# Performance work log

Hardware: AMD Instinct MI355X
Metric: run time of the kernel (lower is better)

The kernel has to match this reference:

```python
import jax, jax.numpy as jnp
import numpy as np

EPS = 1e-5
N, E, G = 65536, 262144, 256
DV, DE, DG = 256, 128, 256


def _ln(x):
    # LayerNorm without affine over the last dim
    mu = jnp.mean(x, axis=-1, keepdims=True)
    var = jnp.mean(jnp.square(x - mu), axis=-1, keepdims=True)
    return (x - mu) * jax.lax.rsqrt(var + EPS)


def setup_inputs() -> dict:
    key = jax.random.key(0)
    ks = jax.random.split(key, 14)
    inp = {
        'fv': jax.random.normal(ks[0], (N, DV), jnp.float32),
        'fe': jax.random.normal(ks[1], (E, DE), jnp.float32),
        'fg': jax.random.normal(ks[2], (G, DG), jnp.float32),
        'fv_pos': jax.random.normal(ks[3], (N, 3), jnp.float32),
        'fv_c': jax.random.normal(ks[4], (N, DV), jnp.float32),
        'fe_c': jax.random.normal(ks[5], (E, DE), jnp.float32),
        'fv_pos_c': jax.random.normal(ks[6], (N, DV), jnp.float32),
        # learned params (original zero-inits the modulation Linears; we use
        # small random weights so the kernel path is exercised)
        'W_v': jax.random.normal(ks[7], (2 * DV, DV), jnp.float32) * 0.02,
        'b_v': jnp.zeros((2 * DV,), jnp.float32),
        'W_vpos': jax.random.normal(ks[8], (DE, DV), jnp.float32) * 0.02,
        'b_vpos': jnp.zeros((DE,), jnp.float32),
        'W_e': jax.random.normal(ks[9], (2 * DE, DE), jnp.float32) * 0.02,
        'b_e': jnp.zeros((2 * DE,), jnp.float32),
        'g_gamma': jnp.ones((DG,), jnp.float32),
        'g_beta': jnp.zeros((DG,), jnp.float32),
        'W_pos': jax.random.normal(ks[10], (1, DG), jnp.float32) * 0.02,
        'b_pos': jnp.zeros((1,), jnp.float32),
        'src': jax.random.randint(ks[11], (E,), 0, N, jnp.int32),
        'dst': jax.random.randint(ks[12], (E,), 0, N, jnp.int32),
        'node_gid': (jnp.arange(N, dtype=jnp.int32) // (N // G)),
    }
    return inp


def reference(fv, fe, fg, fv_pos, fv_c, fe_c, fv_pos_c,
              W_v, b_v, W_vpos, b_vpos, W_e, b_e,
              g_gamma, g_beta, W_pos, b_pos,
              src, dst, node_gid):
    act = jax.nn.silu
    # --- node modulation ---
    mod_v = act(fv_c + fv_pos_c) @ W_v.T + b_v            # [N, 2*DV]
    shift_v, scale_v = jnp.split(mod_v, 2, axis=1)
    fv_out = _ln(fv) * (1.0 + scale_v) + shift_v
    # --- edge modulation with gsddmm('add') gather ---
    fvp = fv_pos_c @ W_vpos.T + b_vpos                    # [N, DE]
    fv2e = fvp[src] + fvp[dst]                            # sddmm add [E, DE]
    mod_e = act(fe_c + fv2e) @ W_e.T + b_e                # [E, 2*DE]
    shift_e, scale_e = jnp.split(mod_e, 2, axis=1)
    fe_out = _ln(fe) * (1.0 + scale_e) + shift_e
    # --- adaptive position scale-norm (per-graph, equivariant) ---
    ones = jnp.ones((N,), fv_pos.dtype)
    cnt = jax.ops.segment_sum(ones, node_gid, num_segments=G)          # [G]
    mean = jax.ops.segment_sum(fv_pos, node_gid, num_segments=G) / cnt[:, None]
    centered = fv_pos - mean[node_gid]                                  # [N, 3]
    sq = jax.ops.segment_sum(jnp.sum(jnp.square(centered), axis=1), node_gid, num_segments=G)
    rms = jnp.sqrt(sq / (cnt * 3.0) + EPS)                              # [G]
    pos_n = centered / rms[node_gid][:, None]
    s = act(fg) @ W_pos.T + b_pos                                       # [G, 1]
    fv_pos_out = pos_n * (1.0 + s)[node_gid]
    # --- graph LayerNorm (affine) ---
    fg_out = _ln(fg) * g_gamma + g_beta
    return (fv_out, fe_out, fg_out, fv_pos_out)
```

## Files before the change

kernel.cpp:

```cpp
#include <hip/hip_runtime.h>

#define N_NODES 65536
#define N_EDGES 262144
#define N_GRAPH 256
#define DV 256
#define DE 128
#define DG 256
#define EPS 1e-5f

typedef __bf16 bf16_t;
typedef bf16_t bf16x8 __attribute__((ext_vector_type(8)));
typedef float f32x4 __attribute__((ext_vector_type(4)));
typedef unsigned short ushort_t;

__device__ __forceinline__ float silu_f(float x) {
  return x / (1.0f + __expf(-x));
}
__device__ __forceinline__ unsigned short f2bf(float f) {
  unsigned int u = __float_as_uint(f);
  u += 0x7fffu + ((u >> 16) & 1u);
  return (unsigned short)(u >> 16);
}
__device__ __forceinline__ float bf2f(unsigned short h) {
  return __uint_as_float(((unsigned int)h) << 16);
}
__device__ __forceinline__ void split_bf(float x, ushort_t& hi, ushort_t& lo) {
  hi = f2bf(x);
  lo = f2bf(x - bf2f(hi));
}
__device__ __forceinline__ void wave_reduce2(float& s1, float& s2) {
  #pragma unroll
  for (int off = 32; off > 0; off >>= 1) {
    s1 += __shfl_xor(s1, off);
    s2 += __shfl_xor(s2, off);
  }
}

__global__ __launch_bounds__(256) void k_prep(
    const float* __restrict__ W_v, const float* __restrict__ W_e,
    const float* __restrict__ W_vpos, ushort_t* __restrict__ Wv_bf,
    ushort_t* __restrict__ We_bf, ushort_t* __restrict__ Wvpos_bf) {
  int idx = blockIdx.x * 256 + threadIdx.x;
  const float* s;
  ushort_t* d;
  int o;
  if (idx < 32768) { s = W_v; d = Wv_bf; o = idx; }
  else if (idx < 40960) { s = W_e; d = We_bf; o = idx - 32768; }
  else { s = W_vpos; d = Wvpos_bf; o = idx - 40960; }
  float4 v = *(const float4*)&s[(size_t)o * 4];
  ushort4 r;
  r.x = f2bf(v.x); r.y = f2bf(v.y); r.z = f2bf(v.z); r.w = f2bf(v.w);
  *(ushort4*)&d[(size_t)o * 4] = r;
}

__global__ __launch_bounds__(512) void k_fvp(
    const float* __restrict__ fv_pos_c, const ushort_t* __restrict__ Wvpos_bf,
    const float* __restrict__ b_vpos, ushort_t* __restrict__ fvp_bf) {
  __shared__ __align__(16) ushort_t Xh[32][264];
  __shared__ __align__(16) ushort_t Xl[32][264];
  const int tid = threadIdx.x;
  const int l = tid & 63, w = tid >> 6;
  const int m0 = blockIdx.x * 32;
  #pragma unroll
  for (int i = 0; i < 4; ++i) {
    int idx = i * 512 + tid;
    int r = idx >> 6, c4 = idx & 63;
    float4 v = *(const float4*)&fv_pos_c[(size_t)(m0 + r) * DV + c4 * 4];
    ushort4 h, lo;
    split_bf(v.x, h.x, lo.x);
    split_bf(v.y, h.y, lo.y);
    split_bf(v.z, h.z, lo.z);
    split_bf(v.w, h.w, lo.w);
    *(ushort4*)&Xh[r][c4 * 4] = h;
    *(ushort4*)&Xl[r][c4 * 4] = lo;
  }
  __syncthreads();
  f32x4 acc[2];
  acc[0] = (f32x4)(0.f);
  acc[1] = (f32x4)(0.f);
  const int mrow = (w & 1) * 16;
  const int ncol0 = (w >> 1) * 32;
  const int arow = mrow + (l & 15);
  for (int kc = 0; kc < 8; ++kc) {
    int ke = kc * 32 + (l >> 4) * 8;
    bf16x8 ah = *(const bf16x8*)&Xh[arow][ke];
    bf16x8 al = *(const bf16x8*)&Xl[arow][ke];
    #pragma unroll
    for (int ni = 0; ni < 2; ++ni) {
      bf16x8 b = *(const bf16x8*)&Wvpos_bf[(size_t)(ncol0 + ni * 16 + (l & 15)) * DV + ke];
      acc[ni] = __builtin_amdgcn_mfma_f32_16x16x32_bf16(al, b, acc[ni], 0, 0, 0);
      acc[ni] = __builtin_amdgcn_mfma_f32_16x16x32_bf16(ah, b, acc[ni], 0, 0, 0);
    }
  }
  #pragma unroll
  for (int ni = 0; ni < 2; ++ni) {
    int col = ncol0 + ni * 16 + (l & 15);
    float bias = b_vpos[col];
    #pragma unroll
    for (int j = 0; j < 4; ++j) {
      int row = m0 + mrow + (l >> 4) * 4 + j;
      fvp_bf[(size_t)row * DE + col] = f2bf(acc[ni][j] + bias);
    }
  }
}

__global__ __launch_bounds__(512) void k_node(
    const float* __restrict__ fv, const float* __restrict__ fv_c,
    const float* __restrict__ fv_pos_c, const ushort_t* __restrict__ Wv_bf,
    const float* __restrict__ b_v, float* __restrict__ fv_out) {
  __shared__ __align__(16) ushort_t Xh[32][264];
  __shared__ __align__(16) ushort_t Xl[32][264];
  __shared__ float muL[32], rsL[32];
  const int tid = threadIdx.x;
  const int l = tid & 63, w = tid >> 6;
  const int m0 = blockIdx.x * 32;
  #pragma unroll
  for (int i = 0; i < 4; ++i) {
    int idx = i * 512 + tid;
    int r = idx >> 6, c4 = idx & 63;
    size_t g = (size_t)(m0 + r) * DV + c4 * 4;
    float4 a = *(const float4*)&fv_c[g];
    float4 b = *(const float4*)&fv_pos_c[g];
    ushort4 h, lo;
    split_bf(silu_f(a.x + b.x), h.x, lo.x);
    split_bf(silu_f(a.y + b.y), h.y, lo.y);
    split_bf(silu_f(a.z + b.z), h.z, lo.z);
    split_bf(silu_f(a.w + b.w), h.w, lo.w);
    *(ushort4*)&Xh[r][c4 * 4] = h;
    *(ushort4*)&Xl[r][c4 * 4] = lo;
  }
  #pragma unroll
  for (int rr = 0; rr < 4; ++rr) {
    int row = w * 4 + rr;
    float4 v = *(const float4*)&fv[(size_t)(m0 + row) * DV + l * 4];
    float s1 = v.x + v.y + v.z + v.w;
    float s2 = v.x * v.x + v.y * v.y + v.z * v.z + v.w * v.w;
    wave_reduce2(s1, s2);
    if (l == 0) {
      float mu = s1 * (1.0f / DV);
      float var = s2 * (1.0f / DV) - mu * mu;
      muL[row] = mu;
      rsL[row] = rsqrtf(var + EPS);
    }
  }
  __syncthreads();
  f32x4 acc[2][4];
  #pragma unroll
  for (int mi = 0; mi < 2; ++mi)
    #pragma unroll
    for (int ni = 0; ni < 4; ++ni) acc[mi][ni] = (f32x4)(0.f);
  int ncol[4];
  ncol[0] = w * 32;
  ncol[1] = w * 32 + 16;
  ncol[2] = DV + w * 32;
  ncol[3] = DV + w * 32 + 16;
  for (int kc = 0; kc < 8; ++kc) {
    int ke = kc * 32 + (l >> 4) * 8;
    bf16x8 ah[2], al[2];
    #pragma unroll
    for (int mi = 0; mi < 2; ++mi) {
      ah[mi] = *(const bf16x8*)&Xh[mi * 16 + (l & 15)][ke];
      al[mi] = *(const bf16x8*)&Xl[mi * 16 + (l & 15)][ke];
    }
    #pragma unroll
    for (int ni = 0; ni < 4; ++ni) {
      bf16x8 b = *(const bf16x8*)&Wv_bf[(size_t)(ncol[ni] + (l & 15)) * DV + ke];
      #pragma unroll
      for (int mi = 0; mi < 2; ++mi) {
        acc[mi][ni] = __builtin_amdgcn_mfma_f32_16x16x32_bf16(al[mi], b, acc[mi][ni], 0, 0, 0);
        acc[mi][ni] = __builtin_amdgcn_mfma_f32_16x16x32_bf16(ah[mi], b, acc[mi][ni], 0, 0, 0);
      }
    }
  }
  #pragma unroll
  for (int ni2 = 0; ni2 < 2; ++ni2) {
    int c = w * 32 + ni2 * 16 + (l & 15);
    float bsh = b_v[c];
    float bsc = b_v[DV + c];
    #pragma unroll
    for (int mi = 0; mi < 2; ++mi)
      #pragma unroll
      for (int j = 0; j < 4; ++j) {
        int row = mi * 16 + (l >> 4) * 4 + j;
        size_t g = (size_t)(m0 + row) * DV + c;
        float v = fv[g];
        float sh = acc[mi][ni2][j] + bsh;
        float sc = acc[mi][ni2 + 2][j] + bsc;
        fv_out[g] = (v - muL[row]) * rsL[row] * (1.0f + sc) + sh;
      }
  }
}

__global__ __launch_bounds__(512) void k_edge(
    const float* __restrict__ fe, const float* __restrict__ fe_c,
    const ushort_t* __restrict__ fvp_bf, const int* __restrict__ src,
    const int* __restrict__ dst, const ushort_t* __restrict__ We_bf,
    const float* __restrict__ b_e, float* __restrict__ fe_out) {
  __shared__ __align__(16) ushort_t Xh[64][136];
  __shared__ __align__(16) ushort_t Xl[64][136];
  __shared__ float muL[64], rsL[64];
  const int tid = threadIdx.x;
  const int l = tid & 63, w = tid >> 6;
  const int m0 = blockIdx.x * 64;
  const int sub = l & 15, quad = l >> 4;
  #pragma unroll
  for (int i = 0; i < 4; ++i) {
    int idx = i * 512 + tid;
    int r = idx >> 5, c4 = idx & 31;
    int sr = src[m0 + r], dr = dst[m0 + r];
    float4 a = *(const float4*)&fe_c[(size_t)(m0 + r) * DE + c4 * 4];
    ushort4 p = *(const ushort4*)&fvp_bf[(size_t)sr * DE + c4 * 4];
    ushort4 q = *(const ushort4*)&fvp_bf[(size_t)dr * DE + c4 * 4];
    ushort4 h, lo;
    split_bf(silu_f(a.x + bf2f(p.x) + bf2f(q.x)), h.x, lo.x);
    split_bf(silu_f(a.y + bf2f(p.y) + bf2f(q.y)), h.y, lo.y);
    split_bf(silu_f(a.z + bf2f(p.z) + bf2f(q.z)), h.z, lo.z);
    split_bf(silu_f(a.w + bf2f(p.w) + bf2f(q.w)), h.w, lo.w);
    *(ushort4*)&Xh[r][c4 * 4] = h;
    *(ushort4*)&Xl[r][c4 * 4] = lo;
  }
  #pragma unroll
  for (int j2 = 0; j2 < 2; ++j2) {
    int row = w * 8 + quad * 2 + j2;
    float s1 = 0.f, s2 = 0.f;
    #pragma unroll
    for (int ci = 0; ci < 8; ++ci) {
      float v = fe[(size_t)(m0 + row) * DE + ci * 16 + sub];
      s1 += v;
      s2 += v * v;
    }
    #pragma unroll
    for (int off = 1; off < 16; off <<= 1) {
      s1 += __shfl_xor(s1, off);
      s2 += __shfl_xor(s2, off);
    }
    if (sub == 0) {
      float m = s1 * (1.0f / DE);
      float var = s2 * (1.0f / DE) - m * m;
      muL[row] = m;
      rsL[row] = rsqrtf(var + EPS);
    }
  }
  __syncthreads();
  f32x4 acc[4][2];
  #pragma unroll
  for (int mi = 0; mi < 4; ++mi) {
    acc[mi][0] = (f32x4)(0.f);
    acc[mi][1] = (f32x4)(0.f);
  }
  for (int kc = 0; kc < 4; ++kc) {
    int ke = kc * 32 + quad * 8;
    bf16x8 ah[4], al[4];
    #pragma unroll
    for (int mi = 0; mi < 4; ++mi) {
      ah[mi] = *(const bf16x8*)&Xh[mi * 16 + sub][ke];
      al[mi] = *(const bf16x8*)&Xl[mi * 16 + sub][ke];
    }
    #pragma unroll
    for (int ni = 0; ni < 2; ++ni) {
      bf16x8 b = *(const bf16x8*)&We_bf[(size_t)(ni * DE + w * 16 + sub) * DE + ke];
      #pragma unroll
      for (int mi = 0; mi < 4; ++mi) {
        acc[mi][ni] = __builtin_amdgcn_mfma_f32_16x16x32_bf16(al[mi], b, acc[mi][ni], 0, 0, 0);
        acc[mi][ni] = __builtin_amdgcn_mfma_f32_16x16x32_bf16(ah[mi], b, acc[mi][ni], 0, 0, 0);
      }
    }
  }
  {
    int c = w * 16 + sub;
    float bsh = b_e[c];
    float bsc = b_e[DE + c];
    #pragma unroll
    for (int mi = 0; mi < 4; ++mi)
      #pragma unroll
      for (int j = 0; j < 4; ++j) {
        int row = mi * 16 + quad * 4 + j;
        size_t g = (size_t)(m0 + row) * DE + c;
        float v = fe[g];
        float sh = acc[mi][0][j] + bsh;
        float sc = acc[mi][1][j] + bsc;
        fe_out[g] = (v - muL[row]) * rsL[row] * (1.0f + sc) + sh;
      }
  }
}

__global__ __launch_bounds__(256) void k_fg_pos(
    const float* __restrict__ fg, const float* __restrict__ g_gamma,
    const float* __restrict__ g_beta, const float* __restrict__ W_pos,
    const float* __restrict__ b_pos, const float* __restrict__ fv_pos,
    const int* __restrict__ node_gid, float* __restrict__ fg_out,
    float* __restrict__ pos_out) {
  const int g = blockIdx.x, t = threadIdx.x;
  const int lane = t & 63, wave = t >> 6;
  __shared__ float p1[4], p2[4], p3[4];
  __shared__ float px[4], py[4], pz[4], pq[4];
  float x = fg[g * DG + t];
  float sv = silu_f(x) * W_pos[t];
  float s1 = x, s2 = x * x, s3 = sv;
  #pragma unroll
  for (int off = 32; off > 0; off >>= 1) {
    s1 += __shfl_xor(s1, off);
    s2 += __shfl_xor(s2, off);
    s3 += __shfl_xor(s3, off);
  }
  if (lane == 0) { p1[wave] = s1; p2[wave] = s2; p3[wave] = s3; }
  __syncthreads();
  s1 = p1[0] + p1[1] + p1[2] + p1[3];
  s2 = p2[0] + p2[1] + p2[2] + p2[3];
  float mu = s1 * (1.0f / DG);
  float var = s2 * (1.0f / DG) - mu * mu;
  float rstd = rsqrtf(var + EPS);
  fg_out[g * DG + t] = (x - mu) * rstd * g_gamma[t] + g_beta[t];
  float s_own = (p3[0] + p3[1] + p3[2] + p3[3]) + b_pos[0];
  const int i = g * 256 + t;
  const int gid = node_gid[i];
  float vx = fv_pos[3 * i + 0];
  float vy = fv_pos[3 * i + 1];
  float vz = fv_pos[3 * i + 2];
  if (__syncthreads_and(gid == g)) {
    float rx = vx, ry = vy, rz = vz, rq = vx * vx + vy * vy + vz * vz;
    #pragma unroll
    for (int off = 32; off > 0; off >>= 1) {
      rx += __shfl_xor(rx, off);
      ry += __shfl_xor(ry, off);
      rz += __shfl_xor(rz, off);
      rq += __shfl_xor(rq, off);
    }
    if (lane == 0) { px[wave] = rx; py[wave] = ry; pz[wave] = rz; pq[wave] = rq; }
    __syncthreads();
    float sx = px[0] + px[1] + px[2] + px[3];
    float sy = py[0] + py[1] + py[2] + py[3];
    float sz = pz[0] + pz[1] + pz[2] + pz[3];
    float sq = pq[0] + pq[1] + pq[2] + pq[3];
    float ic = 1.0f / 256.0f;
    float mx = sx * ic, my = sy * ic, mz = sz * ic;
    float cq = fmaxf(sq - 256.0f * (mx * mx + my * my + mz * mz), 0.0f);
    float rms = sqrtf(cq / (256.0f * 3.0f) + EPS);
    float sc = (1.0f + s_own) / rms;
    pos_out[3 * i + 0] = (vx - mx) * sc;
    pos_out[3 * i + 1] = (vy - my) * sc;
    pos_out[3 * i + 2] = (vz - mz) * sc;
  } else {
    float sx = 0.f, sy = 0.f, sz = 0.f, sq = 0.f, cnt = 0.f;
    for (int j = 0; j < N_NODES; ++j) {
      if (node_gid[j] == gid) {
        float ax = fv_pos[3 * j + 0];
        float ay = fv_pos[3 * j + 1];
        float az = fv_pos[3 * j + 2];
        sx += ax; sy += ay; sz += az;
        sq += ax * ax + ay * ay + az * az;
        cnt += 1.0f;
      }
    }
    float ic = 1.0f / fmaxf(cnt, 1.0f);
    float mx = sx * ic, my = sy * ic, mz = sz * ic;
    float cq = fmaxf(sq - cnt * (mx * mx + my * my + mz * mz), 0.0f);
    float rms = sqrtf(cq / (cnt * 3.0f) + EPS);
    float sg = 0.f;
    for (int c = 0; c < DG; ++c) sg += silu_f(fg[gid * DG + c]) * W_pos[c];
    float sc = (1.0f + sg + b_pos[0]) / rms;
    pos_out[3 * i + 0] = (vx - mx) * sc;
    pos_out[3 * i + 1] = (vy - my) * sc;
    pos_out[3 * i + 2] = (vz - mz) * sc;
  }
}

extern "C" void kernel_launch(void* const* d_in, const int* in_sizes, int n_in,
                              void* d_out, int out_size, void* d_ws,
                              size_t ws_size, hipStream_t stream) {
  const float* fv = (const float*)d_in[0];
  const float* fe = (const float*)d_in[1];
  const float* fg = (const float*)d_in[2];
  const float* fv_pos = (const float*)d_in[3];
  const float* fv_c = (const float*)d_in[4];
  const float* fe_c = (const float*)d_in[5];
  const float* fv_pos_c = (const float*)d_in[6];
  const float* W_v = (const float*)d_in[7];
  const float* b_v = (const float*)d_in[8];
  const float* W_vpos = (const float*)d_in[9];
  const float* b_vpos = (const float*)d_in[10];
  const float* W_e = (const float*)d_in[11];
  const float* b_e = (const float*)d_in[12];
  const float* g_gamma = (const float*)d_in[13];
  const float* g_beta = (const float*)d_in[14];
  const float* W_pos = (const float*)d_in[15];
  const float* b_pos = (const float*)d_in[16];
  const int* src = (const int*)d_in[17];
  const int* dst = (const int*)d_in[18];
  const int* node_gid = (const int*)d_in[19];

  float* out = (float*)d_out;
  float* fv_out = out;
  float* fe_out = fv_out + (size_t)N_NODES * DV;
  float* fg_out = fe_out + (size_t)N_EDGES * DE;
  float* pos_out = fg_out + (size_t)N_GRAPH * DG;

  char* ws = (char*)d_ws;
  ushort_t* fvp_bf = (ushort_t*)ws;
  ushort_t* Wv_bf = (ushort_t*)(ws + 16777216);
  ushort_t* We_bf = (ushort_t*)(ws + 16777216 + 262144);
  ushort_t* Wvpos_bf = (ushort_t*)(ws + 16777216 + 262144 + 65536);

  k_prep<<<192, 256, 0, stream>>>(W_v, W_e, W_vpos, Wv_bf, We_bf, Wvpos_bf);
  k_fvp<<<N_NODES / 32, 512, 0, stream>>>(fv_pos_c, Wvpos_bf, b_vpos, fvp_bf);
  k_node<<<N_NODES / 32, 512, 0, stream>>>(fv, fv_c, fv_pos_c, Wv_bf, b_v, fv_out);
  k_edge<<<N_EDGES / 64, 512, 0, stream>>>(fe, fe_c, fvp_bf, src, dst, We_bf,
                                           b_e, fe_out);
  k_fg_pos<<<N_GRAPH, 256, 0, stream>>>(fg, g_gamma, g_beta, W_pos, b_pos,
                                        fv_pos, node_gid, fg_out, pos_out);
}
```

Measured before the change: 274.1 us.

## Merge node and edge modulation kernels into one interleaved launch

Fuses the node and edge modulation kernels into a single launch of 6144 blocks. Each group of three blocks handles one 32-row node tile and two 64-row edge tiles, with both paths sharing one shared-memory buffer. This removes a launch and the tail and ramp gap between the two kernels, and lets node and edge work run on the GPU at the same time. In exchange, shared-memory use per block is now the larger of the two layouts, which may lower occupancy for the node path, and the branch per block makes blocks uneven in cost.

```diff
diff --git a/kernel.cpp b/kernel.cpp
--- a/kernel.cpp
+++ b/kernel.cpp
@@ -104,183 +104,186 @@
   }
 }
 
-__global__ __launch_bounds__(512) void k_node(
+__global__ __launch_bounds__(512) void k_node_edge(
     const float* __restrict__ fv, const float* __restrict__ fv_c,
     const float* __restrict__ fv_pos_c, const ushort_t* __restrict__ Wv_bf,
-    const float* __restrict__ b_v, float* __restrict__ fv_out) {
-  __shared__ __align__(16) ushort_t Xh[32][264];
-  __shared__ __align__(16) ushort_t Xl[32][264];
-  __shared__ float muL[32], rsL[32];
-  const int tid = threadIdx.x;
-  const int l = tid & 63, w = tid >> 6;
-  const int m0 = blockIdx.x * 32;
-  #pragma unroll
-  for (int i = 0; i < 4; ++i) {
-    int idx = i * 512 + tid;
-    int r = idx >> 6, c4 = idx & 63;
-    size_t g = (size_t)(m0 + r) * DV + c4 * 4;
-    float4 a = *(const float4*)&fv_c[g];
-    float4 b = *(const float4*)&fv_pos_c[g];
-    ushort4 h, lo;
-    split_bf(silu_f(a.x + b.x), h.x, lo.x);
-    split_bf(silu_f(a.y + b.y), h.y, lo.y);
-    split_bf(silu_f(a.z + b.z), h.z, lo.z);
-    split_bf(silu_f(a.w + b.w), h.w, lo.w);
-    *(ushort4*)&Xh[r][c4 * 4] = h;
-    *(ushort4*)&Xl[r][c4 * 4] = lo;
-  }
-  #pragma unroll
-  for (int rr = 0; rr < 4; ++rr) {
-    int row = w * 4 + rr;
-    float4 v = *(const float4*)&fv[(size_t)(m0 + row) * DV + l * 4];
-    float s1 = v.x + v.y + v.z + v.w;
-    float s2 = v.x * v.x + v.y * v.y + v.z * v.z + v.w * v.w;
-    wave_reduce2(s1, s2);
-    if (l == 0) {
-      float mu = s1 * (1.0f / DV);
-      float var = s2 * (1.0f / DV) - mu * mu;
-      muL[row] = mu;
-      rsL[row] = rsqrtf(var + EPS);
-    }
-  }
-  __syncthreads();
-  f32x4 acc[2][4];
-  #pragma unroll
-  for (int mi = 0; mi < 2; ++mi)
-    #pragma unroll
-    for (int ni = 0; ni < 4; ++ni) acc[mi][ni] = (f32x4)(0.f);
-  int ncol[4];
-  ncol[0] = w * 32;
-  ncol[1] = w * 32 + 16;
-  ncol[2] = DV + w * 32;
-  ncol[3] = DV + w * 32 + 16;
-  for (int kc = 0; kc < 8; ++kc) {
-    int ke = kc * 32 + (l >> 4) * 8;
-    bf16x8 ah[2], al[2];
-    #pragma unroll
-    for (int mi = 0; mi < 2; ++mi) {
-      ah[mi] = *(const bf16x8*)&Xh[mi * 16 + (l & 15)][ke];
-      al[mi] = *(const bf16x8*)&Xl[mi * 16 + (l & 15)][ke];
-    }
-    #pragma unroll
-    for (int ni = 0; ni < 4; ++ni) {
-      bf16x8 b = *(const bf16x8*)&Wv_bf[(size_t)(ncol[ni] + (l & 15)) * DV + ke];
-      #pragma unroll
-      for (int mi = 0; mi < 2; ++mi) {
-        acc[mi][ni] = __builtin_amdgcn_mfma_f32_16x16x32_bf16(al[mi], b, acc[mi][ni], 0, 0, 0);
-        acc[mi][ni] = __builtin_amdgcn_mfma_f32_16x16x32_bf16(ah[mi], b, acc[mi][ni], 0, 0, 0);
-      }
-    }
-  }
-  #pragma unroll
-  for (int ni2 = 0; ni2 < 2; ++ni2) {
-    int c = w * 32 + ni2 * 16 + (l & 15);
-    float bsh = b_v[c];
-    float bsc = b_v[DV + c];
-    #pragma unroll
-    for (int mi = 0; mi < 2; ++mi)
-      #pragma unroll
-      for (int j = 0; j < 4; ++j) {
-        int row = mi * 16 + (l >> 4) * 4 + j;
-        size_t g = (size_t)(m0 + row) * DV + c;
-        float v = fv[g];
-        float sh = acc[mi][ni2][j] + bsh;
-        float sc = acc[mi][ni2 + 2][j] + bsc;
-        fv_out[g] = (v - muL[row]) * rsL[row] * (1.0f + sc) + sh;
-      }
-  }
-}
-
-__global__ __launch_bounds__(512) void k_edge(
+    const float* __restrict__ b_v, float* __restrict__ fv_out,
     const float* __restrict__ fe, const float* __restrict__ fe_c,
     const ushort_t* __restrict__ fvp_bf, const int* __restrict__ src,
     const int* __restrict__ dst, const ushort_t* __restrict__ We_bf,
     const float* __restrict__ b_e, float* __restrict__ fe_out) {
-  __shared__ __align__(16) ushort_t Xh[64][136];
-  __shared__ __align__(16) ushort_t Xl[64][136];
-  __shared__ float muL[64], rsL[64];
+  __shared__ __align__(16) char smem[35328];
+  const int bid = blockIdx.x;
+  const int g3 = bid / 3, r3 = bid % 3;
   const int tid = threadIdx.x;
   const int l = tid & 63, w = tid >> 6;
-  const int m0 = blockIdx.x * 64;
-  const int sub = l & 15, quad = l >> 4;
-  #pragma unroll
-  for (int i = 0; i < 4; ++i) {
-    int idx = i * 512 + tid;
-    int r = idx >> 5, c4 = idx & 31;
-    int sr = src[m0 + r], dr = dst[m0 + r];
-    float4 a = *(const float4*)&fe_c[(size_t)(m0 + r) * DE + c4 * 4];
-    ushort4 p = *(const ushort4*)&fvp_bf[(size_t)sr * DE + c4 * 4];
-    ushort4 q = *(const ushort4*)&fvp_bf[(size_t)dr * DE + c4 * 4];
-    ushort4 h, lo;
-    split_bf(silu_f(a.x + bf2f(p.x) + bf2f(q.x)), h.x, lo.x);
-    split_bf(silu_f(a.y + bf2f(p.y) + bf2f(q.y)), h.y, lo.y);
-    split_bf(silu_f(a.z + bf2f(p.z) + bf2f(q.z)), h.z, lo.z);
-    split_bf(silu_f(a.w + bf2f(p.w) + bf2f(q.w)), h.w, lo.w);
-    *(ushort4*)&Xh[r][c4 * 4] = h;
-    *(ushort4*)&Xl[r][c4 * 4] = lo;
-  }
-  #pragma unroll
-  for (int j2 = 0; j2 < 2; ++j2) {
-    int row = w * 8 + quad * 2 + j2;
-    float s1 = 0.f, s2 = 0.f;
-    #pragma unroll
-    for (int ci = 0; ci < 8; ++ci) {
-      float v = fe[(size_t)(m0 + row) * DE + ci * 16 + sub];
-      s1 += v;
-      s2 += v * v;
-    }
-    #pragma unroll
-    for (int off = 1; off < 16; off <<= 1) {
-      s1 += __shfl_xor(s1, off);
-      s2 += __shfl_xor(s2, off);
-    }
-    if (sub == 0) {
-      float m = s1 * (1.0f / DE);
-      float var = s2 * (1.0f / DE) - m * m;
-      muL[row] = m;
-      rsL[row] = rsqrtf(var + EPS);
-    }
-  }
-  __syncthreads();
-  f32x4 acc[4][2];
-  #pragma unroll
-  for (int mi = 0; mi < 4; ++mi) {
-    acc[mi][0] = (f32x4)(0.f);
-    acc[mi][1] = (f32x4)(0.f);
-  }
-  for (int kc = 0; kc < 4; ++kc) {
-    int ke = kc * 32 + quad * 8;
-    bf16x8 ah[4], al[4];
+  if (r3 == 0) {
+    ushort_t (*Xh)[264] = (ushort_t(*)[264])smem;
+    ushort_t (*Xl)[264] = (ushort_t(*)[264])(smem + 16896);
+    float* muL = (float*)(smem + 33792);
+    float* rsL = (float*)(smem + 33920);
+    const int m0 = g3 * 32;
+    #pragma unroll
+    for (int i = 0; i < 4; ++i) {
+      int idx = i * 512 + tid;
+      int r = idx >> 6, c4 = idx & 63;
+      size_t g = (size_t)(m0 + r) * DV + c4 * 4;
+      float4 a = *(const float4*)&fv_c[g];
+      float4 b = *(const float4*)&fv_pos_c[g];
+      ushort4 h, lo;
+      split_bf(silu_f(a.x + b.x), h.x, lo.x);
+      split_bf(silu_f(a.y + b.y), h.y, lo.y);
+      split_bf(silu_f(a.z + b.z), h.z, lo.z);
+      split_bf(silu_f(a.w + b.w), h.w, lo.w);
+      *(ushort4*)&Xh[r][c4 * 4] = h;
+      *(ushort4*)&Xl[r][c4 * 4] = lo;
+    }
+    #pragma unroll
+    for (int rr = 0; rr < 4; ++rr) {
+      int row = w * 4 + rr;
+      float4 v = *(const float4*)&fv[(size_t)(m0 + row) * DV + l * 4];
+      float s1 = v.x + v.y + v.z + v.w;
+      float s2 = v.x * v.x + v.y * v.y + v.z * v.z + v.w * v.w;
+      wave_reduce2(s1, s2);
+      if (l == 0) {
+        float mu = s1 * (1.0f / DV);
+        float var = s2 * (1.0f / DV) - mu * mu;
+        muL[row] = mu;
+        rsL[row] = rsqrtf(var + EPS);
+      }
+    }
+    __syncthreads();
+    f32x4 acc[2][4];
+    #pragma unroll
+    for (int mi = 0; mi < 2; ++mi)
+      #pragma unroll
+      for (int ni = 0; ni < 4; ++ni) acc[mi][ni] = (f32x4)(0.f);
+    int ncol[4];
+    ncol[0] = w * 32;
+    ncol[1] = w * 32 + 16;
+    ncol[2] = DV + w * 32;
+    ncol[3] = DV + w * 32 + 16;
+    for (int kc = 0; kc < 8; ++kc) {
+      int ke = kc * 32 + (l >> 4) * 8;
+      bf16x8 ah[2], al[2];
+      #pragma unroll
+      for (int mi = 0; mi < 2; ++mi) {
+        ah[mi] = *(const bf16x8*)&Xh[mi * 16 + (l & 15)][ke];
+        al[mi] = *(const bf16x8*)&Xl[mi * 16 + (l & 15)][ke];
+      }
+      #pragma unroll
+      for (int ni = 0; ni < 4; ++ni) {
+        bf16x8 b = *(const bf16x8*)&Wv_bf[(size_t)(ncol[ni] + (l & 15)) * DV + ke];
+        #pragma unroll
+        for (int mi = 0; mi < 2; ++mi) {
+          acc[mi][ni] = __builtin_amdgcn_mfma_f32_16x16x32_bf16(al[mi], b, acc[mi][ni], 0, 0, 0);
+          acc[mi][ni] = __builtin_amdgcn_mfma_f32_16x16x32_bf16(ah[mi], b, acc[mi][ni], 0, 0, 0);
+        }
+      }
+    }
+    #pragma unroll
+    for (int ni2 = 0; ni2 < 2; ++ni2) {
+      int c = w * 32 + ni2 * 16 + (l & 15);
+      float bsh = b_v[c];
+      float bsc = b_v[DV + c];
+      #pragma unroll
+      for (int mi = 0; mi < 2; ++mi)
+        #pragma unroll
+        for (int j = 0; j < 4; ++j) {
+          int row = mi * 16 + (l >> 4) * 4 + j;
+          size_t g = (size_t)(m0 + row) * DV + c;
+          float v = fv[g];
+          float sh = acc[mi][ni2][j] + bsh;
+          float sc = acc[mi][ni2 + 2][j] + bsc;
+          fv_out[g] = (v - muL[row]) * rsL[row] * (1.0f + sc) + sh;
+        }
+    }
+  } else {
+    ushort_t (*Xh)[136] = (ushort_t(*)[136])smem;
+    ushort_t (*Xl)[136] = (ushort_t(*)[136])(smem + 17408);
+    float* muL = (float*)(smem + 34816);
+    float* rsL = (float*)(smem + 35072);
+    const int m0 = (g3 * 2 + (r3 - 1)) * 64;
+    const int sub = l & 15, quad = l >> 4;
+    #pragma unroll
+    for (int i = 0; i < 4; ++i) {
+      int idx = i * 512 + tid;
+      int r = idx >> 5, c4 = idx & 31;
+      int sr = src[m0 + r], dr = dst[m0 + r];
+      float4 a = *(const float4*)&fe_c[(size_t)(m0 + r) * DE + c4 * 4];
+      ushort4 p = *(const ushort4*)&fvp_bf[(size_t)sr * DE + c4 * 4];
+      ushort4 q = *(const ushort4*)&fvp_bf[(size_t)dr * DE + c4 * 4];
+      ushort4 h, lo;
+      split_bf(silu_f(a.x + bf2f(p.x) + bf2f(q.x)), h.x, lo.x);
+      split_bf(silu_f(a.y + bf2f(p.y) + bf2f(q.y)), h.y, lo.y);
+      split_bf(silu_f(a.z + bf2f(p.z) + bf2f(q.z)), h.z, lo.z);
+      split_bf(silu_f(a.w + bf2f(p.w) + bf2f(q.w)), h.w, lo.w);
+      *(ushort4*)&Xh[r][c4 * 4] = h;
+      *(ushort4*)&Xl[r][c4 * 4] = lo;
+    }
+    #pragma unroll
+    for (int j2 = 0; j2 < 2; ++j2) {
+      int row = w * 8 + quad * 2 + j2;
+      float s1 = 0.f, s2 = 0.f;
+      #pragma unroll
+      for (int ci = 0; ci < 8; ++ci) {
+        float v = fe[(size_t)(m0 + row) * DE + ci * 16 + sub];
+        s1 += v;
+        s2 += v * v;
+      }
+      #pragma unroll
+      for (int off = 1; off < 16; off <<= 1) {
+        s1 += __shfl_xor(s1, off);
+        s2 += __shfl_xor(s2, off);
+      }
+      if (sub == 0) {
+        float m = s1 * (1.0f / DE);
+        float var = s2 * (1.0f / DE) - m * m;
+        muL[row] = m;
+        rsL[row] = rsqrtf(var + EPS);
+      }
+    }
+    __syncthreads();
+    f32x4 acc[4][2];
     #pragma unroll
     for (int mi = 0; mi < 4; ++mi) {
-      ah[mi] = *(const bf16x8*)&Xh[mi * 16 + sub][ke];
-      al[mi] = *(const bf16x8*)&Xl[mi * 16 + sub][ke];
-    }
-    #pragma unroll
-    for (int ni = 0; ni < 2; ++ni) {
-      bf16x8 b = *(const bf16x8*)&We_bf[(size_t)(ni * DE + w * 16 + sub) * DE + ke];
+      acc[mi][0] = (f32x4)(0.f);
+      acc[mi][1] = (f32x4)(0.f);
+    }
+    for (int kc = 0; kc < 4; ++kc) {
+      int ke = kc * 32 + quad * 8;
+      bf16x8 ah[4], al[4];
       #pragma unroll
       for (int mi = 0; mi < 4; ++mi) {
-        acc[mi][ni] = __builtin_amdgcn_mfma_f32_16x16x32_bf16(al[mi], b, acc[mi][ni], 0, 0, 0);
-        acc[mi][ni] = __builtin_amdgcn_mfma_f32_16x16x32_bf16(ah[mi], b, acc[mi][ni], 0, 0, 0);
-      }
-    }
-  }
-  {
-    int c = w * 16 + sub;
-    float bsh = b_e[c];
-    float bsc = b_e[DE + c];
-    #pragma unroll
-    for (int mi = 0; mi < 4; ++mi)
-      #pragma unroll
-      for (int j = 0; j < 4; ++j) {
-        int row = mi * 16 + quad * 4 + j;
-        size_t g = (size_t)(m0 + row) * DE + c;
-        float v = fe[g];
-        float sh = acc[mi][0][j] + bsh;
-        float sc = acc[mi][1][j] + bsc;
-        fe_out[g] = (v - muL[row]) * rsL[row] * (1.0f + sc) + sh;
-      }
+        ah[mi] = *(const bf16x8*)&Xh[mi * 16 + sub][ke];
+        al[mi] = *(const bf16x8*)&Xl[mi * 16 + sub][ke];
+      }
+      #pragma unroll
+      for (int ni = 0; ni < 2; ++ni) {
+        bf16x8 b = *(const bf16x8*)&We_bf[(size_t)(ni * DE + w * 16 + sub) * DE + ke];
+        #pragma unroll
+        for (int mi = 0; mi < 4; ++mi) {
+          acc[mi][ni] = __builtin_amdgcn_mfma_f32_16x16x32_bf16(al[mi], b, acc[mi][ni], 0, 0, 0);
+          acc[mi][ni] = __builtin_amdgcn_mfma_f32_16x16x32_bf16(ah[mi], b, acc[mi][ni], 0, 0, 0);
+        }
+      }
+    }
+    {
+      int c = w * 16 + sub;
+      float bsh = b_e[c];
+      float bsc = b_e[DE + c];
+      #pragma unroll
+      for (int mi = 0; mi < 4; ++mi)
+        #pragma unroll
+        for (int j = 0; j < 4; ++j) {
+          int row = mi * 16 + quad * 4 + j;
+          size_t g = (size_t)(m0 + row) * DE + c;
+          float v = fe[g];
+          float sh = acc[mi][0][j] + bsh;
+          float sc = acc[mi][1][j] + bsc;
+          fe_out[g] = (v - muL[row]) * rsL[row] * (1.0f + sc) + sh;
+        }
+    }
   }
 }
 
@@ -403,9 +406,9 @@
 
   k_prep<<<192, 256, 0, stream>>>(W_v, W_e, W_vpos, Wv_bf, We_bf, Wvpos_bf);
   k_fvp<<<N_NODES / 32, 512, 0, stream>>>(fv_pos_c, Wvpos_bf, b_vpos, fvp_bf);
-  k_node<<<N_NODES / 32, 512, 0, stream>>>(fv, fv_c, fv_pos_c, Wv_bf, b_v, fv_out);
-  k_edge<<<N_EDGES / 64, 512, 0, stream>>>(fe, fe_c, fvp_bf, src, dst, We_bf,
-                                           b_e, fe_out);
+  k_node_edge<<<6144, 512, 0, stream>>>(fv, fv_c, fv_pos_c, Wv_bf, b_v, fv_out,
+                                        fe, fe_c, fvp_bf, src, dst, We_bf,
+                                        b_e, fe_out);
   k_fg_pos<<<N_GRAPH, 256, 0, stream>>>(fg, g_gamma, g_beta, W_pos, b_pos,
                                         fv_pos, node_gid, fg_out, pos_out);
 }
```

Result: slower. 314.7 us (+14.8%).
